# Optimization experiments

Measured on AMD Instinct MI355X. Metric: run time of the kernel, lower is better.

## Reference

```python
import jax, jax.numpy as jnp
import numpy as np


def setup_inputs() -> dict:
    key = jax.random.key(0)
    ks = jax.random.split(key, 5)
    B, S, D, H, DK, DV = 4, 2048, 1024, 16, 64, 64
    return {
        "x": jax.random.normal(ks[0], (B, S, D), dtype=jnp.float32),
        "W_q": jax.random.normal(ks[1], (H, D, DK), dtype=jnp.float32),
        "W_k": jax.random.normal(ks[2], (H, D, DK), dtype=jnp.float32),
        "W_v": jax.random.normal(ks[3], (H, D, DV), dtype=jnp.float32),
        "W_0": jax.random.normal(ks[4], (DV * H, D), dtype=jnp.float32),
    }


def reference(x, W_q, W_k, W_v, W_0):
    # x: [B, S, D]; W_q/W_k: [H, D, DK]; W_v: [H, D, DV]; W_0: [H*DV, D]
    B, S, D = x.shape
    H, _, DK = W_q.shape
    DV = W_v.shape[-1]
    Q = jnp.einsum("bsd,hdk->bhsk", x, W_q)
    K = jnp.einsum("bsd,hdk->bhsk", x, W_k)
    V = jnp.einsum("bsd,hdv->bhsv", x, W_v)
    scale = 1.0 / jnp.sqrt(jnp.asarray(DK, x.dtype))
    score = jnp.einsum("bhqk,bhsk->bhqs", Q, K) * scale  # [B,H,S,S]
    causal = jnp.tril(jnp.ones((S, S), dtype=bool))
    score = jnp.where(causal, score, -jnp.inf)
    attn = jax.nn.softmax(score, axis=-1)
    heads = jnp.einsum("bhqs,bhsv->bhqv", attn, V)  # [B,H,S,DV]
    # torch.cat along last dim in head order == transpose heads next to DV
    heads = heads.transpose(0, 2, 1, 3).reshape(B, S, H * DV)
    return heads @ W_0
```

## Files before the change

### kernel.cpp

```cpp
#include <hip/hip_runtime.h>

typedef __bf16 bf16;
typedef __bf16 bf16x4 __attribute__((ext_vector_type(4)));
typedef __bf16 bf16x8 __attribute__((ext_vector_type(8)));
typedef float  f32x2  __attribute__((ext_vector_type(2)));
typedef float  f32x4  __attribute__((ext_vector_type(4)));

#define NEG_INF (-__builtin_inff())
#define L2E 1.44269504088896f
#define DEFER_THR 5.545177444479562f

__device__ __forceinline__ void gl16(const void* g, void* l) {
    __builtin_amdgcn_global_load_lds(
        (const __attribute__((address_space(1))) void*)g,
        (__attribute__((address_space(3))) void*)l, 16, 0, 0);
}

__global__ void k_split_x(const float* __restrict__ x,
                          bf16* __restrict__ xh, bf16* __restrict__ xl) {
    int i = (blockIdx.x * 256 + threadIdx.x) * 4;
    float4 v = *reinterpret_cast<const float4*>(x + i);
    float a[4] = {v.x, v.y, v.z, v.w};
    bf16x4 h, l;
    #pragma unroll
    for (int e = 0; e < 4; e++) {
        bf16 hh = (bf16)a[e];
        h[e] = hh;
        l[e] = (bf16)(a[e] - (float)hh);
    }
    *reinterpret_cast<bf16x4*>(xh + i) = h;
    *reinterpret_cast<bf16x4*>(xl + i) = l;
}


__global__ void k_cvt_wqkv(const float* __restrict__ wq, const float* __restrict__ wk,
                           const float* __restrict__ wv,
                           bf16* __restrict__ ohi, bf16* __restrict__ olo) {
    __shared__ float tile[64][65];
    const int d0 = blockIdx.x * 64, h = blockIdx.y, proj = blockIdx.z;
    const float* w = (proj == 0) ? wq : ((proj == 1) ? wk : wv);
    const int t = threadIdx.x;
    {
        int k = t & 63, dr = t >> 6;
        #pragma unroll
        for (int i = 0; i < 16; i++) {
            int dl = i * 4 + dr;
            tile[dl][k] = w[(size_t)(h * 1024 + d0 + dl) * 64 + k];
        }
    }
    __syncthreads();
    {
        int dl = t & 63, kr = t >> 6;
        #pragma unroll
        for (int i = 0; i < 16; i++) {
            int k = i * 4 + kr;
            float v = tile[dl][k];
            bf16 hi = (bf16)v;
            size_t o = (size_t)(proj * 1024 + h * 64 + k) * 1024 + d0 + dl;
            ohi[o] = hi;
            olo[o] = (bf16)(v - (float)hi);
        }
    }
}

__global__ void k_cvt_w0(const float* __restrict__ w0, bf16* __restrict__ out) {
    __shared__ float tile[64][65];
    const int n0 = blockIdx.x * 64, c0 = blockIdx.y * 64;
    const int t = threadIdx.x;
    {
        int n = t & 63, cr = t >> 6;
        #pragma unroll
        for (int i = 0; i < 16; i++) {
            int cl = i * 4 + cr;
            tile[cl][n] = w0[(size_t)(c0 + cl) * 1024 + n0 + n];
        }
    }
    __syncthreads();
    {
        int cl = t & 63, nr = t >> 6;
        #pragma unroll
        for (int i = 0; i < 16; i++) {
            int nl = i * 4 + nr;
            out[(size_t)(n0 + nl) * 1024 + c0 + cl] = (bf16)tile[cl][nl];
        }
    }
}

__global__ __launch_bounds__(256)
void k_gemm3(const bf16* __restrict__ Ah, const bf16* __restrict__ Al,
             const bf16* __restrict__ Bh, const bf16* __restrict__ Bl,
             bf16* __restrict__ Qhi, bf16* __restrict__ Qlo,
             bf16* __restrict__ Khi, bf16* __restrict__ Klo)
{
    __shared__ char LDS[65536];
    const int t = threadIdx.x;
    const int m0 = blockIdx.x * 128;
    const int n0 = blockIdx.y * 128;
    const int wid = t >> 6, lane = t & 63, lr = lane & 15, lg = lane >> 4;
    const int wm = wid >> 1, wn = wid & 1;

    const int eoff = (lane >> 3) * 1024 + (((lane & 7) ^ (lane >> 3)) * 8);
    const bf16* pAh = Ah + (size_t)m0 * 1024 + eoff;
    const bf16* pAl = Al + (size_t)m0 * 1024 + eoff;
    const bf16* pBh = Bh + (size_t)n0 * 1024 + eoff;
    const bf16* pBl = Bl + (size_t)n0 * 1024 + eoff;

    f32x4 acc[4][4] = {};

    for (int k0 = 0; k0 < 1024; k0 += 64) {
        #pragma unroll
        for (int i = 0; i < 4; i++) {
            const int r0 = (wid * 4 + i) * 8;
            const size_t gofs = (size_t)r0 * 1024 + k0;
            char* ld = LDS + r0 * 128;
            gl16(pAh + gofs, ld);
            gl16(pAl + gofs, ld + 16384);
            gl16(pBh + gofs, ld + 32768);
            gl16(pBl + gofs, ld + 49152);
        }
        __syncthreads();
        #pragma unroll
        for (int kk = 0; kk < 2; kk++) {
            bf16x8 ah[4], al[4], bh[4], bl[4];
            #pragma unroll
            for (int mt = 0; mt < 4; mt++) {
                int row = wm * 64 + mt * 16 + lr;
                int off = row * 128 + (((kk * 4 + lg) * 16) ^ ((row & 7) << 4));
                ah[mt] = *reinterpret_cast<const bf16x8*>(LDS + off);
                al[mt] = *reinterpret_cast<const bf16x8*>(LDS + 16384 + off);
            }
            #pragma unroll
            for (int nt = 0; nt < 4; nt++) {
                int row = wn * 64 + nt * 16 + lr;
                int off = row * 128 + (((kk * 4 + lg) * 16) ^ ((row & 7) << 4));
                bh[nt] = *reinterpret_cast<const bf16x8*>(LDS + 32768 + off);
                bl[nt] = *reinterpret_cast<const bf16x8*>(LDS + 49152 + off);
            }
            #pragma unroll
            for (int mt = 0; mt < 4; mt++)
                #pragma unroll
                for (int nt = 0; nt < 4; nt++) {
                    acc[mt][nt] = __builtin_amdgcn_mfma_f32_16x16x32_bf16(
                        ah[mt], bh[nt], acc[mt][nt], 0, 0, 0);
                    acc[mt][nt] = __builtin_amdgcn_mfma_f32_16x16x32_bf16(
                        ah[mt], bl[nt], acc[mt][nt], 0, 0, 0);
                    acc[mt][nt] = __builtin_amdgcn_mfma_f32_16x16x32_bf16(
                        al[mt], bh[nt], acc[mt][nt], 0, 0, 0);
                }
        }
        __syncthreads();
    }

    #pragma unroll
    for (int mt = 0; mt < 4; mt++)
        #pragma unroll
        for (int nt = 0; nt < 4; nt++)
            #pragma unroll
            for (int j = 0; j < 4; j++) {
                int m = m0 + wm * 64 + mt * 16 + lg * 4 + j;
                int n = n0 + wn * 64 + nt * 16 + lr;
                float v = acc[mt][nt][j];
                int b = m >> 11, s = m & 2047;
                if (n < 1024) {
                    int h = n >> 6, k = n & 63;
                    size_t idx = ((size_t)(b * 16 + h) * 2048 + s) * 64 + k;
                    float vs = v * 0.125f;
                    bf16 hi = (bf16)vs;
                    Qhi[idx] = hi;
                    Qlo[idx] = (bf16)(vs - (float)hi);
                } else {
                    int n2 = n - 1024, h = n2 >> 6, k = n2 & 63;
                    size_t idx = ((size_t)(b * 16 + h) * 2048 + s) * 64 + k;
                    bf16 hi = (bf16)v;
                    Khi[idx] = hi;
                    Klo[idx] = (bf16)(v - (float)hi);
                }
            }
}

template<int MODE>
__global__ __launch_bounds__(256)
void k_gemm2(const bf16* __restrict__ A, const bf16* __restrict__ Bt,
             bf16* __restrict__ Vtb, float* __restrict__ Out)
{
    __shared__ char LDS[32768];
    const int t = threadIdx.x;
    const int m0 = blockIdx.x * 128;
    const int n0 = blockIdx.y * 128;
    const int wid = t >> 6, lane = t & 63, lr = lane & 15, lg = lane >> 4;
    const int wm = wid >> 1, wn = wid & 1;

    const int eoff = (lane >> 3) * 1024 + (((lane & 7) ^ (lane >> 3)) * 8);
    const bf16* pA = A + (size_t)m0 * 1024 + eoff;
    const bf16* pB = Bt + (size_t)n0 * 1024 + eoff;

    f32x4 acc[4][4] = {};

    for (int k0 = 0; k0 < 1024; k0 += 64) {
        #pragma unroll
        for (int i = 0; i < 4; i++) {
            const int r0 = (wid * 4 + i) * 8;
            const size_t gofs = (size_t)r0 * 1024 + k0;
            char* ld = LDS + r0 * 128;
            gl16(pA + gofs, ld);
            gl16(pB + gofs, ld + 16384);
        }
        __syncthreads();
        #pragma unroll
        for (int kk = 0; kk < 2; kk++) {
            bf16x8 af[4], bfr[4];
            #pragma unroll
            for (int mt = 0; mt < 4; mt++) {
                int row = wm * 64 + mt * 16 + lr;
                af[mt] = *reinterpret_cast<const bf16x8*>(
                    LDS + row * 128 + (((kk * 4 + lg) * 16) ^ ((row & 7) << 4)));
            }
            #pragma unroll
            for (int nt = 0; nt < 4; nt++) {
                int row = wn * 64 + nt * 16 + lr;
                bfr[nt] = *reinterpret_cast<const bf16x8*>(
                    LDS + 16384 + row * 128 + (((kk * 4 + lg) * 16) ^ ((row & 7) << 4)));
            }
            #pragma unroll
            for (int mt = 0; mt < 4; mt++)
                #pragma unroll
                for (int nt = 0; nt < 4; nt++)
                    acc[mt][nt] = __builtin_amdgcn_mfma_f32_16x16x32_bf16(
                        af[mt], bfr[nt], acc[mt][nt], 0, 0, 0);
        }
        __syncthreads();
    }

    #pragma unroll
    for (int mt = 0; mt < 4; mt++)
        #pragma unroll
        for (int nt = 0; nt < 4; nt++)
            #pragma unroll
            for (int j = 0; j < 4; j++) {
                int m = m0 + wm * 64 + mt * 16 + lg * 4 + j;
                int nl = n0 + wn * 64 + nt * 16 + lr;
                if (MODE == 0) {
                    int b = m >> 11, s = m & 2047;
                    int h = nl >> 6, dv = nl & 63;
                    Vtb[((size_t)(b * 16 + h) * 64 + dv) * 2048 + s] = (bf16)acc[mt][nt][j];
                } else {
                    Out[(size_t)m * 1024 + nl] = acc[mt][nt][j];
                }
            }
}

__global__ __launch_bounds__(512, 4)
void k_attn(const bf16* __restrict__ Qhi, const bf16* __restrict__ Qlo,
            const bf16* __restrict__ Khi, const bf16* __restrict__ Klo,
            const bf16* __restrict__ Vtb, bf16* __restrict__ hd)
{
    __shared__ char LDS[49152];
    const int bid = blockIdx.x;
    const int x7 = bid & 7, k6 = bid >> 3;
    const int hh = k6 >> 3, pr = k6 & 7;
    const int bh = x7 * 8 + hh;
    const int t = threadIdx.x, wid = t >> 6, lane = t & 63, lr = lane & 15, lg = lane >> 4;
    const bf16* Qhp = Qhi + (size_t)bh * 131072;
    const bf16* Qlp = Qlo + (size_t)bh * 131072;
    const bf16* Kbase = Khi + (size_t)bh * 131072;
    const bf16* Lbase = Klo + (size_t)bh * 131072;
    const bf16* Vbase = Vtb + (size_t)bh * 131072;

    const int swc = (lr & 7) << 4;
    const int b0 = lr * 128 + ((lg * 16) ^ swc);
    const int b1 = lr * 128 + ((64 + lg * 16) ^ swc);

    const int r = t >> 3, c8 = t & 7;
    const int wb = r * 128 + ((c8 * 16) ^ ((r & 7) << 4));
    const int koff = r * 64 + c8 * 8;
    const int voff = r * 2048 + c8 * 8;

    #pragma unroll 1
    for (int pass = 0; pass < 2; pass++) {
        const int qB = pass ? pr : 15 - pr;
        const int q0 = qB * 128 + wid * 16;
        const int qdiv = q0 >> 6;
        const int kbmax = 2 * qB + 1;
        const int qg = q0 + lr;

        bf16x8 qh[2], ql[2];
        #pragma unroll
        for (int kk = 0; kk < 2; kk++) {
            size_t off = (size_t)(q0 + lr) * 64 + kk * 32 + lg * 8;
            qh[kk] = *reinterpret_cast<const bf16x8*>(Qhp + off);
            ql[kk] = *reinterpret_cast<const bf16x8*>(Qlp + off);
        }

        const bf16* gk = Kbase + koff;
        const bf16* gl = Lbase + koff;
        const bf16* gv = Vbase + voff;

        {
            bf16x8 a = *reinterpret_cast<const bf16x8*>(gk);
            bf16x8 b = *reinterpret_cast<const bf16x8*>(gl);
            bf16x8 c = *reinterpret_cast<const bf16x8*>(gv);
            *reinterpret_cast<bf16x8*>(LDS + wb) = a;
            *reinterpret_cast<bf16x8*>(LDS + wb + 8192) = b;
            *reinterpret_cast<bf16x8*>(LDS + wb + 16384) = c;
        }
        __syncthreads();

        f32x4 accO[4] = {};
        float mrow = NEG_INF;
        float negmL2 = NEG_INF;
        f32x2 lsum2 = {0.0f, 0.0f};

        for (int kb = 0; kb <= kbmax; kb++) {
            const int ro = (kb & 1) ? 24576 : 0;
            const int wo = 24576 - ro;
            bf16x8 pkh, pkl, pv;
            if (kb < kbmax) {
                gk += 4096; gl += 4096; gv += 64;
                pkh = *reinterpret_cast<const bf16x8*>(gk);
                pkl = *reinterpret_cast<const bf16x8*>(gl);
                pv  = *reinterpret_cast<const bf16x8*>(gv);
            }

            if (kb <= qdiv) {
                const int bA = b0 + ro, bB = b1 + ro;
                f32x4 sc[4] = {};
                __builtin_amdgcn_s_setprio(1);
                #pragma unroll
                for (int kk = 0; kk < 2; kk++) {
                    const int bb = kk ? bB : bA;
                    bf16x8 bh8[4], bl8[4];
                    #pragma unroll
                    for (int nt = 0; nt < 4; nt++) {
                        bh8[nt] = *reinterpret_cast<const bf16x8*>(LDS + bb + nt * 2048);
                        bl8[nt] = *reinterpret_cast<const bf16x8*>(LDS + bb + nt * 2048 + 8192);
                    }
                    #pragma unroll
                    for (int nt = 0; nt < 4; nt++) {
                        sc[nt] = __builtin_amdgcn_mfma_f32_16x16x32_bf16(bh8[nt], qh[kk], sc[nt], 0, 0, 0);
                        sc[nt] = __builtin_amdgcn_mfma_f32_16x16x32_bf16(bl8[nt], qh[kk], sc[nt], 0, 0, 0);
                        sc[nt] = __builtin_amdgcn_mfma_f32_16x16x32_bf16(bh8[nt], ql[kk], sc[nt], 0, 0, 0);
                    }
                }
                __builtin_amdgcn_s_setprio(0);

                if (kb == qdiv) {
                    #pragma unroll
                    for (int nt = 0; nt < 4; nt++)
                        #pragma unroll
                        for (int j = 0; j < 4; j++) {
                            int kg = kb * 64 + nt * 16 + 4 * lg + j;
                            if (kg > qg) sc[nt][j] = NEG_INF;
                        }
                }

                float mA = fmaxf(fmaxf(sc[0][0], sc[0][1]), sc[0][2]);
                float mB = fmaxf(fmaxf(sc[0][3], sc[1][0]), sc[1][1]);
                float mC = fmaxf(fmaxf(sc[1][2], sc[1][3]), sc[2][0]);
                float mD = fmaxf(fmaxf(sc[2][1], sc[2][2]), sc[2][3]);
                float mE = fmaxf(fmaxf(sc[3][0], sc[3][1]), sc[3][2]);
                float lm = fmaxf(fmaxf(fmaxf(mA, mB), fmaxf(mC, mD)),
                                 fmaxf(mE, sc[3][3]));
                if (__any(lm > mrow + DEFER_THR)) {
                    float pm = lm;
                    pm = fmaxf(pm, __shfl_xor(pm, 16));
                    pm = fmaxf(pm, __shfl_xor(pm, 32));
                    float mnew = fmaxf(mrow, pm);
                    float alpha = __builtin_amdgcn_exp2f((mrow - mnew) * L2E);
                    mrow = mnew;
                    negmL2 = -mnew * L2E;
                    lsum2 *= alpha;
                    #pragma unroll
                    for (int nt = 0; nt < 4; nt++)
                        #pragma unroll
                        for (int j = 0; j < 4; j++)
                            accO[nt][j] *= alpha;
                }

                f32x2 pr2[8];
                #pragma unroll
                for (int nt = 0; nt < 4; nt++) {
                    pr2[2 * nt]     = __builtin_shufflevector(sc[nt], sc[nt], 0, 1);
                    pr2[2 * nt + 1] = __builtin_shufflevector(sc[nt], sc[nt], 2, 3);
                }
                const f32x2 vL2E = {L2E, L2E};
                const f32x2 vneg = {negmL2, negmL2};
                f32x2 ts2 = {0.0f, 0.0f};
                #pragma unroll
                for (int i = 0; i < 8; i++) {
                    f32x2 a = __builtin_elementwise_fma(pr2[i], vL2E, vneg);
                    f32x2 e;
                    e.x = __builtin_amdgcn_exp2f(a.x);
                    e.y = __builtin_amdgcn_exp2f(a.y);
                    pr2[i] = e;
                    ts2 += e;
                }
                lsum2 += ts2;

                unsigned int w[4][2];
                #pragma unroll
                for (int nt = 0; nt < 4; nt++)
                    #pragma unroll
                    for (int p = 0; p < 2; p++) {
                        unsigned int d;
                        asm("v_cvt_pk_bf16_f32 %0, %1, %2"
                            : "=v"(d) : "v"(pr2[2 * nt + p].x), "v"(pr2[2 * nt + p].y));
                        w[nt][p] = d;
                    }
                bf16x8 bp[2];
                #pragma unroll
                for (int kk = 0; kk < 2; kk++) {
                    unsigned int a0 = w[2 * kk][0], bq0 = w[2 * kk + 1][0];
                    unsigned int a1 = w[2 * kk][1], bq1 = w[2 * kk + 1][1];
                    asm("v_permlane32_swap_b32 %0, %1" : "+v"(a0), "+v"(bq0));
                    asm("v_permlane16_swap_b32 %0, %1" : "+v"(a0), "+v"(bq0));
                    asm("v_permlane32_swap_b32 %0, %1" : "+v"(a1), "+v"(bq1));
                    asm("v_permlane16_swap_b32 %0, %1" : "+v"(a1), "+v"(bq1));
                    union { unsigned int u[4]; bf16x8 v; } cvt;
                    cvt.u[0] = a0; cvt.u[1] = a1; cvt.u[2] = bq0; cvt.u[3] = bq1;
                    bp[kk] = cvt.v;
                }

                __builtin_amdgcn_s_setprio(1);
                #pragma unroll
                for (int kk = 0; kk < 2; kk++) {
                    const int bb = kk ? bB : bA;
                    #pragma unroll
                    for (int nt = 0; nt < 4; nt++) {
                        bf16x8 bv = *reinterpret_cast<const bf16x8*>(LDS + bb + nt * 2048 + 16384);
                        accO[nt] = __builtin_amdgcn_mfma_f32_16x16x32_bf16(bv, bp[kk], accO[nt], 0, 0, 0);
                    }
                }
                __builtin_amdgcn_s_setprio(0);
            }

            if (kb < kbmax) {
                *reinterpret_cast<bf16x8*>(LDS + wb + wo) = pkh;
                *reinterpret_cast<bf16x8*>(LDS + wb + wo + 8192) = pkl;
                *reinterpret_cast<bf16x8*>(LDS + wb + wo + 16384) = pv;
            }
            __syncthreads();
        }

        float ps = lsum2.x + lsum2.y;
        ps += __shfl_xor(ps, 16);
        ps += __shfl_xor(ps, 32);
        float inv = 1.0f / ps;
        size_t rowbase = (size_t)((bh >> 4) * 2048 + qg) * 1024 + (bh & 15) * 64;
        #pragma unroll
        for (int nt = 0; nt < 4; nt++) {
            bf16x4 o;
            #pragma unroll
            for (int j = 0; j < 4; j++) o[j] = (bf16)(accO[nt][j] * inv);
            *reinterpret_cast<bf16x4*>(hd + rowbase + nt * 16 + 4 * lg) = o;
        }
    }
}


extern "C" void kernel_launch(void* const* d_in, const int* in_sizes, int n_in,
                              void* d_out, int out_size, void* d_ws, size_t ws_size,
                              hipStream_t stream) {
    const float* x  = (const float*)d_in[0];
    const float* Wq = (const float*)d_in[1];
    const float* Wk = (const float*)d_in[2];
    const float* Wv = (const float*)d_in[3];
    const float* W0 = (const float*)d_in[4];
    float* out = (float*)d_out;

    char* ws = (char*)d_ws;
    bf16* w0t = (bf16*)(ws + 0);
    bf16* Qhi = (bf16*)(ws + 2097152);
    bf16* Qlo = (bf16*)(ws + 18874368);
    bf16* Khi = (bf16*)(ws + 35651584);
    bf16* Klo = (bf16*)(ws + 52428800);
    bf16* Vtb = (bf16*)(ws + 69206016);
    bf16* whi = (bf16*)(ws + 85983232);
    bf16* wlo = (bf16*)(ws + 92274688);
    bf16* hd  = (bf16*)(ws + 85983232);
    if (ws_size < 102760448u) return;

    bf16* xh = (bf16*)d_out;
    bf16* xl = xh + 8388608;

    k_split_x <<<8192, 256, 0, stream>>>(x, xh, xl);
    k_cvt_wqkv<<<dim3(16, 16, 3), 256, 0, stream>>>(Wq, Wk, Wv, whi, wlo);
    k_cvt_w0  <<<dim3(16, 16), 256, 0, stream>>>(W0, w0t);
    k_gemm3   <<<dim3(64, 16), 256, 0, stream>>>(xh, xl, whi, wlo, Qhi, Qlo, Khi, Klo);
    k_gemm2<0><<<dim3(64, 8), 256, 0, stream>>>(xh, whi + 2048 * 1024, Vtb, nullptr);
    k_attn    <<<512, 512, 0, stream>>>(Qhi, Qlo, Khi, Klo, Vtb, hd);
    k_gemm2<1><<<dim3(64, 8), 256, 0, stream>>>(hd, w0t, nullptr, out);
}
```

Baseline: 244.4 us.

## Double-buffer LDS tiles in projection GEMMs with K=32 steps and MFMA priority

Both projection GEMM kernels now use a ping-pong LDS buffer with a K-step of 32 instead of 64. The global-to-LDS loads for the next step are issued before the MFMAs on the current buffer, leaving one barrier per iteration instead of two. The swizzle is adapted to the 64-byte row stride, and s_setprio raises wave priority around the MFMA block. This is meant to hide global load latency behind compute, at the cost of twice as many loop iterations and barriers.

```diff
diff --git a/kernel.cpp b/kernel.cpp
--- a/kernel.cpp
+++ b/kernel.cpp
@@ -14,6 +14,9 @@
     __builtin_amdgcn_global_load_lds(
         (const __attribute__((address_space(1))) void*)g,
         (__attribute__((address_space(3))) void*)l, 16, 0, 0);
+}
+__device__ __forceinline__ bf16x8 ld128(const char* p) {
+    return *reinterpret_cast<const bf16x8*>(p);
 }
 
 __global__ void k_split_x(const float* __restrict__ x,
@@ -99,55 +102,72 @@
     const int wid = t >> 6, lane = t & 63, lr = lane & 15, lg = lane >> 4;
     const int wm = wid >> 1, wn = wid & 1;
 
-    const int eoff = (lane >> 3) * 1024 + (((lane & 7) ^ (lane >> 3)) * 8);
+    const int rr = lane >> 2, sl = lane & 3;
+    const int eoff = rr * 1024 + ((sl ^ ((rr >> 1) & 3)) * 8);
     const bf16* pAh = Ah + (size_t)m0 * 1024 + eoff;
     const bf16* pAl = Al + (size_t)m0 * 1024 + eoff;
     const bf16* pBh = Bh + (size_t)n0 * 1024 + eoff;
     const bf16* pBl = Bl + (size_t)n0 * 1024 + eoff;
 
+    const int rb = lr * 64 + ((lg ^ ((lr >> 1) & 3)) << 4);
+
     f32x4 acc[4][4] = {};
 
-    for (int k0 = 0; k0 < 1024; k0 += 64) {
-        #pragma unroll
-        for (int i = 0; i < 4; i++) {
-            const int r0 = (wid * 4 + i) * 8;
-            const size_t gofs = (size_t)r0 * 1024 + k0;
-            char* ld = LDS + r0 * 128;
-            gl16(pAh + gofs, ld);
-            gl16(pAl + gofs, ld + 16384);
-            gl16(pBh + gofs, ld + 32768);
-            gl16(pBl + gofs, ld + 49152);
-        }
-        __syncthreads();
-        #pragma unroll
-        for (int kk = 0; kk < 2; kk++) {
-            bf16x8 ah[4], al[4], bh[4], bl[4];
-            #pragma unroll
-            for (int mt = 0; mt < 4; mt++) {
-                int row = wm * 64 + mt * 16 + lr;
-                int off = row * 128 + (((kk * 4 + lg) * 16) ^ ((row & 7) << 4));
-                ah[mt] = *reinterpret_cast<const bf16x8*>(LDS + off);
-                al[mt] = *reinterpret_cast<const bf16x8*>(LDS + 16384 + off);
-            }
+    #pragma unroll
+    for (int i = 0; i < 2; i++) {
+        const int r0 = wid * 32 + i * 16;
+        const size_t g = (size_t)r0 * 1024;
+        char* ld = LDS + r0 * 64;
+        gl16(pAh + g, ld);
+        gl16(pAl + g, ld + 8192);
+        gl16(pBh + g, ld + 16384);
+        gl16(pBl + g, ld + 24576);
+    }
+    __syncthreads();
+
+    for (int ks = 0; ks < 32; ks++) {
+        const int ro = (ks & 1) << 15;
+        const int wo = 32768 - ro;
+        if (ks < 31) {
+            const int k0 = (ks + 1) * 32;
+            #pragma unroll
+            for (int i = 0; i < 2; i++) {
+                const int r0 = wid * 32 + i * 16;
+                const size_t g = (size_t)r0 * 1024 + k0;
+                char* ld = LDS + wo + r0 * 64;
+                gl16(pAh + g, ld);
+                gl16(pAl + g, ld + 8192);
+                gl16(pBh + g, ld + 16384);
+                gl16(pBl + g, ld + 24576);
+            }
+        }
+        bf16x8 ah[4], al[4], bh[4], bl[4];
+        const int base = ro + rb;
+        #pragma unroll
+        for (int mt = 0; mt < 4; mt++) {
+            const int off = base + (wm * 64 + mt * 16) * 64;
+            ah[mt] = ld128(LDS + off);
+            al[mt] = ld128(LDS + off + 8192);
+        }
+        #pragma unroll
+        for (int nt = 0; nt < 4; nt++) {
+            const int off = base + (wn * 64 + nt * 16) * 64;
+            bh[nt] = ld128(LDS + off + 16384);
+            bl[nt] = ld128(LDS + off + 24576);
+        }
+        __builtin_amdgcn_s_setprio(1);
+        #pragma unroll
+        for (int mt = 0; mt < 4; mt++)
             #pragma unroll
             for (int nt = 0; nt < 4; nt++) {
-                int row = wn * 64 + nt * 16 + lr;
-                int off = row * 128 + (((kk * 4 + lg) * 16) ^ ((row & 7) << 4));
-                bh[nt] = *reinterpret_cast<const bf16x8*>(LDS + 32768 + off);
-                bl[nt] = *reinterpret_cast<const bf16x8*>(LDS + 49152 + off);
-            }
-            #pragma unroll
-            for (int mt = 0; mt < 4; mt++)
-                #pragma unroll
-                for (int nt = 0; nt < 4; nt++) {
-                    acc[mt][nt] = __builtin_amdgcn_mfma_f32_16x16x32_bf16(
-                        ah[mt], bh[nt], acc[mt][nt], 0, 0, 0);
-                    acc[mt][nt] = __builtin_amdgcn_mfma_f32_16x16x32_bf16(
-                        ah[mt], bl[nt], acc[mt][nt], 0, 0, 0);
-                    acc[mt][nt] = __builtin_amdgcn_mfma_f32_16x16x32_bf16(
-                        al[mt], bh[nt], acc[mt][nt], 0, 0, 0);
-                }
-        }
+                acc[mt][nt] = __builtin_amdgcn_mfma_f32_16x16x32_bf16(
+                    ah[mt], bh[nt], acc[mt][nt], 0, 0, 0);
+                acc[mt][nt] = __builtin_amdgcn_mfma_f32_16x16x32_bf16(
+                    ah[mt], bl[nt], acc[mt][nt], 0, 0, 0);
+                acc[mt][nt] = __builtin_amdgcn_mfma_f32_16x16x32_bf16(
+                    al[mt], bh[nt], acc[mt][nt], 0, 0, 0);
+            }
+        __builtin_amdgcn_s_setprio(0);
         __syncthreads();
     }
 
@@ -190,44 +210,54 @@
     const int wid = t >> 6, lane = t & 63, lr = lane & 15, lg = lane >> 4;
     const int wm = wid >> 1, wn = wid & 1;
 
-    const int eoff = (lane >> 3) * 1024 + (((lane & 7) ^ (lane >> 3)) * 8);
+    const int rr = lane >> 2, sl = lane & 3;
+    const int eoff = rr * 1024 + ((sl ^ ((rr >> 1) & 3)) * 8);
     const bf16* pA = A + (size_t)m0 * 1024 + eoff;
     const bf16* pB = Bt + (size_t)n0 * 1024 + eoff;
+    const int rb = lr * 64 + ((lg ^ ((lr >> 1) & 3)) << 4);
 
     f32x4 acc[4][4] = {};
 
-    for (int k0 = 0; k0 < 1024; k0 += 64) {
-        #pragma unroll
-        for (int i = 0; i < 4; i++) {
-            const int r0 = (wid * 4 + i) * 8;
-            const size_t gofs = (size_t)r0 * 1024 + k0;
-            char* ld = LDS + r0 * 128;
-            gl16(pA + gofs, ld);
-            gl16(pB + gofs, ld + 16384);
-        }
-        __syncthreads();
-        #pragma unroll
-        for (int kk = 0; kk < 2; kk++) {
-            bf16x8 af[4], bfr[4];
-            #pragma unroll
-            for (int mt = 0; mt < 4; mt++) {
-                int row = wm * 64 + mt * 16 + lr;
-                af[mt] = *reinterpret_cast<const bf16x8*>(
-                    LDS + row * 128 + (((kk * 4 + lg) * 16) ^ ((row & 7) << 4)));
-            }
-            #pragma unroll
-            for (int nt = 0; nt < 4; nt++) {
-                int row = wn * 64 + nt * 16 + lr;
-                bfr[nt] = *reinterpret_cast<const bf16x8*>(
-                    LDS + 16384 + row * 128 + (((kk * 4 + lg) * 16) ^ ((row & 7) << 4)));
-            }
-            #pragma unroll
-            for (int mt = 0; mt < 4; mt++)
-                #pragma unroll
-                for (int nt = 0; nt < 4; nt++)
-                    acc[mt][nt] = __builtin_amdgcn_mfma_f32_16x16x32_bf16(
-                        af[mt], bfr[nt], acc[mt][nt], 0, 0, 0);
-        }
+    #pragma unroll
+    for (int i = 0; i < 2; i++) {
+        const int r0 = wid * 32 + i * 16;
+        const size_t g = (size_t)r0 * 1024;
+        char* ld = LDS + r0 * 64;
+        gl16(pA + g, ld);
+        gl16(pB + g, ld + 8192);
+    }
+    __syncthreads();
+
+    for (int ks = 0; ks < 32; ks++) {
+        const int ro = (ks & 1) << 14;
+        const int wo = 16384 - ro;
+        if (ks < 31) {
+            const int k0 = (ks + 1) * 32;
+            #pragma unroll
+            for (int i = 0; i < 2; i++) {
+                const int r0 = wid * 32 + i * 16;
+                const size_t g = (size_t)r0 * 1024 + k0;
+                char* ld = LDS + wo + r0 * 64;
+                gl16(pA + g, ld);
+                gl16(pB + g, ld + 8192);
+            }
+        }
+        bf16x8 af[4], bfr[4];
+        const int base = ro + rb;
+        #pragma unroll
+        for (int mt = 0; mt < 4; mt++)
+            af[mt] = ld128(LDS + base + (wm * 64 + mt * 16) * 64);
+        #pragma unroll
+        for (int nt = 0; nt < 4; nt++)
+            bfr[nt] = ld128(LDS + base + (wn * 64 + nt * 16) * 64 + 8192);
+        __builtin_amdgcn_s_setprio(1);
+        #pragma unroll
+        for (int mt = 0; mt < 4; mt++)
+            #pragma unroll
+            for (int nt = 0; nt < 4; nt++)
+                acc[mt][nt] = __builtin_amdgcn_mfma_f32_16x16x32_bf16(
+                    af[mt], bfr[nt], acc[mt][nt], 0, 0, 0);
+        __builtin_amdgcn_s_setprio(0);
         __syncthreads();
     }
 
```

Measured after the change: 254.4 us. 4.1% more time.
